# Kernel tuning notes

Measured on AMD Instinct MI355X. Metric: run time of the kernel, lower is better.

## Reference

```python
import jax, jax.numpy as jnp
import numpy as np

GROUPS = 9  # hardcoded in GTLModuleV1.forward


def setup_inputs() -> dict:
    key = jax.random.key(0)
    k1, k2, k3 = jax.random.split(key, 3)
    B, C, N, K = 4, 144, 16384, 16
    queryandkey = jax.random.normal(k1, (B, C, N), dtype=jnp.float32)
    value = jax.random.normal(k2, (B, C, N), dtype=jnp.float32)
    idx_knn = jax.random.randint(k3, (B, N, K), 0, N, dtype=jnp.int32)
    return {"queryandkey": queryandkey, "value": value, "idx_knn": idx_knn}


def _gather_neighbours(x, idx_flat, B, G, d, N, K):
    # x: (B, G, d, N); idx_flat: (B, 1, 1, N*K) -> (B, G, d, N, K)
    g = jnp.take_along_axis(x, jnp.broadcast_to(idx_flat, (B, G, d, N * K)), axis=3)
    return g.reshape(B, G, d, N, K)


def reference(queryandkey, value, idx_knn):
    B, C, N = queryandkey.shape
    K = idx_knn.shape[-1]
    G = GROUPS
    d = C // G  # Cl = C (Cnl = 0 in GTLModuleV1)

    q = queryandkey.reshape(B, G, d, N)          # LocalQuery == LocalKey source
    v = value.reshape(B, G, d, N)
    idx_flat = idx_knn.reshape(B, 1, 1, N * K)

    key_g = _gather_neighbours(q, idx_flat, B, G, d, N, K)  # (B,G,d,N,K)
    val_g = _gather_neighbours(v, idx_flat, B, G, d, N, K)  # (B,G,d,N,K)

    # LocalAtt = sum_d Q * K_gathered, softmax over neighbors
    att = jnp.einsum('bgdn,bgdnk->bgnk', q, key_g)
    att = jax.nn.softmax(att, axis=-1)                       # (B,G,N,K)

    # attention centrality: scatter_add of attention weights onto neighbor ids
    cent = jnp.zeros((B, G, N), dtype=att.dtype).at[
        jnp.arange(B)[:, None, None, None],
        jnp.arange(G)[None, :, None, None],
        idx_knn[:, None, :, :],
    ].add(att)                                               # (B,G,N)

    # weighted aggregation of gathered values
    feat = jnp.einsum('bgnk,bgdnk->bgdn', att, val_g).reshape(B, C, N)
    return feat, cent
```

## Files before the change

kernel.cpp:

```cpp
#include <hip/hip_runtime.h>
#include <hip/hip_fp16.h>

#define BATCH 4
#define CHAN  144
#define NPTS  16384
#define KNN   16
#define GRP   9
#define DIM   16
#define ROWU  (GRP * DIM)
#define PCHUNK 21
#define NPAIR (BATCH * GRP)

#define TT 32

typedef __attribute__((ext_vector_type(2))) _Float16 h2v;
typedef __attribute__((ext_vector_type(4))) float f4v;
typedef __attribute__((ext_vector_type(4))) int   i4v;
__device__ __forceinline__ h2v as_h2(unsigned int u) {
  union { unsigned int u; h2v h; } c; c.u = u; return c.h;
}

template<int J>
__device__ __forceinline__ int ibcast(int v) {
  return __builtin_amdgcn_update_dpp(0, v, (J) * 0x55, 0xF, 0xF, true);
}
template<int C>
__device__ __forceinline__ float fxor(float x) {
  int r = __builtin_amdgcn_update_dpp(0, __builtin_bit_cast(int, x), C, 0xF, 0xF, true);
  return __builtin_bit_cast(float, r);
}

__global__ __launch_bounds__(256) void pack_qv_kernel(
    const float* __restrict__ q, const float* __restrict__ v,
    unsigned int* __restrict__ qvT) {
  __shared__ float tq[TT][TT + 1];
  __shared__ float tv[TT][TT + 1];
  const int b = blockIdx.z;
  const float* qb = q + (size_t)b * CHAN * NPTS;
  const float* vb = v + (size_t)b * CHAN * NPTS;
  unsigned int* out = qvT + (size_t)b * NPTS * ROWU;
  const int n0 = blockIdx.x * TT;
  const int c0 = blockIdx.y * TT;
  const int t = threadIdx.x;

  {
    const int cl = t >> 3, nq = (t & 7) * 4;
    const int c = c0 + cl;
    if (c < CHAN) {
      const float4 a = *(const float4*)&qb[(size_t)c * NPTS + n0 + nq];
      tq[cl][nq + 0] = a.x; tq[cl][nq + 1] = a.y;
      tq[cl][nq + 2] = a.z; tq[cl][nq + 3] = a.w;
      const float4 w = *(const float4*)&vb[(size_t)c * NPTS + n0 + nq];
      tv[cl][nq + 0] = w.x; tv[cl][nq + 1] = w.y;
      tv[cl][nq + 2] = w.z; tv[cl][nq + 3] = w.w;
    }
  }
  __syncthreads();
  {
    const int nl = t >> 3, cq = (t & 7) * 4;
    const int c = c0 + cq;
    if (c < CHAN) {
      const int g = c >> 4, r = c & 15;
      __half2 k01 = __halves2half2(__float2half_rn(tq[cq + 0][nl]),
                                   __float2half_rn(tq[cq + 1][nl]));
      __half2 v01 = __halves2half2(__float2half_rn(tv[cq + 0][nl]),
                                   __float2half_rn(tv[cq + 1][nl]));
      __half2 k23 = __halves2half2(__float2half_rn(tq[cq + 2][nl]),
                                   __float2half_rn(tq[cq + 3][nl]));
      __half2 v23 = __halves2half2(__float2half_rn(tv[cq + 2][nl]),
                                   __float2half_rn(tv[cq + 3][nl]));
      *(uint4*)&out[(size_t)(n0 + nl) * ROWU + g * 16 + r] =
          make_uint4(*(unsigned int*)&k01, *(unsigned int*)&v01,
                     *(unsigned int*)&k23, *(unsigned int*)&v23);
    }
  }
}

__global__ __launch_bounds__(512, 4) void gtl_kernel(
    const unsigned int* __restrict__ qvT,
    const int*   __restrict__ idx,
    float* __restrict__ feat,
    float* __restrict__ part)
{
  const int i = blockIdx.x;
  const int x = i & 7, sblk = i >> 3;
  if (sblk >= 94 + ((x & 1) ^ 1)) return;
  int pair, chunk;
  if (sblk < 84) { pair = x + 8 * (sblk / PCHUNK); chunk = sblk % PCHUNK; }
  else           { pair = 32 + (x >> 1); chunk = (sblk - 84) + 11 * (x & 1); }
  const int b = pair / GRP;
  const int g = pair - b * GRP;

  __shared__ float lcent[NPTS];
  const int tid = threadIdx.x;

  f4v* l4 = (f4v*)lcent;
  #pragma unroll
  for (int ii = 0; ii < NPTS / 4 / 512; ++ii)
    l4[ii * 512 + tid] = (f4v){0.f, 0.f, 0.f, 0.f};
  __syncthreads();

  const int ngroups = 6 + (chunk < 2 ? 1 : 0);
  const int gstart  = 6 * chunk + (chunk < 2 ? chunk : 2);

  const int lane = tid & 63;
  const int wv   = tid >> 6;
  const int slot = lane >> 2;
  const int d    = lane & 3;

  const char* qvb  = (const char*)qvT + (size_t)b * NPTS * (ROWU * 4);
  const char* idxB = (const char*)idx + (size_t)b * NPTS * (KNN * 4);
  const unsigned laneB  = (unsigned)(g * 64 + d * 16);
  const unsigned idxoff = (unsigned)(d * 16);

  int n = gstart * 128 + wv * 16 + slot;
  i4v idq = __builtin_nontemporal_load(
      (const i4v*)(idxB + (unsigned)n * 64u + idxoff));
  uint4 qq = *(const uint4*)(qvb + (unsigned)n * (ROWU * 4u) + laneB);

  for (int it = 0; it < ngroups; ++it) {
    const h2v q01 = as_h2(qq.x);
    const h2v q23 = as_h2(qq.z);

    uint4 kvp[KNN];
#define GSTEP(K)                                                             \
    {                                                                        \
      const int mk = ibcast<((K) >> 2)>(                                     \
          ((K) & 3) == 0 ? idq.x : ((K) & 3) == 1 ? idq.y                    \
                         : ((K) & 3) == 2 ? idq.z : idq.w);                  \
      kvp[K] = *(const uint4*)(qvb + (unsigned)mk * (ROWU * 4u) + laneB);    \
    }
    GSTEP(0)  GSTEP(1)  GSTEP(2)  GSTEP(3)
    GSTEP(4)  GSTEP(5)  GSTEP(6)  GSTEP(7)
    GSTEP(8)  GSTEP(9)  GSTEP(10) GSTEP(11)
    GSTEP(12) GSTEP(13) GSTEP(14) GSTEP(15)
#undef GSTEP

    const int itn = (it + 1 < ngroups) ? it + 1 : it;
    const int nn = (gstart + itn) * 128 + wv * 16 + slot;
    const i4v idqn = __builtin_nontemporal_load(
        (const i4v*)(idxB + (unsigned)nn * 64u + idxoff));
    const uint4 qqn = *(const uint4*)(qvb + (unsigned)nn * (ROWU * 4u) + laneB);

    __builtin_amdgcn_sched_barrier(0);

    float p[KNN];
    float sum = 0.f, a0 = 0.f, a1 = 0.f, a2 = 0.f, a3 = 0.f;
#define CSTEP(K)                                                             \
    {                                                                        \
      float s = __builtin_amdgcn_fdot2(as_h2(kvp[K].x), q01, 0.f, false);    \
      s = __builtin_amdgcn_fdot2(as_h2(kvp[K].z), q23, s, false);            \
      s += fxor<0xB1>(s);                                                    \
      s += fxor<0x4E>(s);                                                    \
      const float e = __expf(s);                                             \
      p[K] = e; sum += e;                                                    \
      const float2 v01 = __half22float2(*(const __half2*)&kvp[K].y);         \
      const float2 v23 = __half22float2(*(const __half2*)&kvp[K].w);         \
      a0 += e * v01.x; a1 += e * v01.y; a2 += e * v23.x; a3 += e * v23.y;    \
    }
    CSTEP(0)  CSTEP(1)  CSTEP(2)  CSTEP(3)
    CSTEP(4)  CSTEP(5)  CSTEP(6)  CSTEP(7)
    CSTEP(8)  CSTEP(9)  CSTEP(10) CSTEP(11)
    CSTEP(12) CSTEP(13) CSTEP(14) CSTEP(15)
#undef CSTEP

    const float inv = 1.f / sum;

    const float w0 = (d == 0 ? p[0] : d == 1 ? p[4] : d == 2 ? p[8]  : p[12]) * inv;
    const float w1 = (d == 0 ? p[1] : d == 1 ? p[5] : d == 2 ? p[9]  : p[13]) * inv;
    const float w2 = (d == 0 ? p[2] : d == 1 ? p[6] : d == 2 ? p[10] : p[14]) * inv;
    const float w3 = (d == 0 ? p[3] : d == 1 ? p[7] : d == 2 ? p[11] : p[15]) * inv;
    atomicAdd(&lcent[idq.x], w0);
    atomicAdd(&lcent[idq.y], w1);
    atomicAdd(&lcent[idq.z], w2);
    atomicAdd(&lcent[idq.w], w3);

    float* fb = feat + ((size_t)b * CHAN + g * DIM + 4 * d) * NPTS + n;
    __builtin_nontemporal_store(a0 * inv, fb);
    __builtin_nontemporal_store(a1 * inv, fb + NPTS);
    __builtin_nontemporal_store(a2 * inv, fb + 2 * NPTS);
    __builtin_nontemporal_store(a3 * inv, fb + 3 * NPTS);

    n = nn; idq = idqn; qq = qqn;
  }

  __syncthreads();
  f4v* p4 = (f4v*)(part + ((size_t)pair * PCHUNK + chunk) * NPTS);
  #pragma unroll
  for (int i2 = 0; i2 < NPTS / 4 / 512; ++i2)
    __builtin_nontemporal_store(l4[i2 * 512 + tid], &p4[i2 * 512 + tid]);
}

__global__ __launch_bounds__(256) void reduce_cent_kernel(
    const float* __restrict__ part, float* __restrict__ cent) {
  const int t = blockIdx.x * 256 + threadIdx.x;
  const int bg = t >> 12;
  const int m4 = (t & 4095) << 2;
  const f4v* p = (const f4v*)(part + ((size_t)bg * PCHUNK) * NPTS + m4);
  f4v s = (f4v){0.f, 0.f, 0.f, 0.f};
  #pragma unroll
  for (int i = 0; i < PCHUNK; ++i) {
    f4v xv = __builtin_nontemporal_load(&p[(size_t)i * (NPTS / 4)]);
    s += xv;
  }
  *(f4v*)(cent + (size_t)bg * NPTS + m4) = s;
}

extern "C" void kernel_launch(void* const* d_in, const int* in_sizes, int n_in,
                              void* d_out, int out_size, void* d_ws, size_t ws_size,
                              hipStream_t stream) {
  const float* q   = (const float*)d_in[0];
  const float* v   = (const float*)d_in[1];
  const int*   idx = (const int*)d_in[2];

  float* feat = (float*)d_out;
  float* cent = feat + (size_t)BATCH * CHAN * NPTS;

  unsigned int* qvT = (unsigned int*)d_ws;
  float* part = (float*)(qvT + (size_t)BATCH * NPTS * ROWU);

  dim3 tg(NPTS / TT, (CHAN + TT - 1) / TT, BATCH);
  pack_qv_kernel<<<tg, 256, 0, stream>>>(q, v, qvT);

  gtl_kernel<<<760, 512, 0, stream>>>(qvT, idx, feat, part);

  reduce_cent_kernel<<<(NPAIR * NPTS / 4) / 256, 256, 0, stream>>>(part, cent);
}
```

Baseline: 226.5 us.

## Replace partial-centrality buffer and reduce kernel with global atomic accumulation

New measurement: 234.3 us. 3.4% more time.

```diff
diff --git a/kernel.cpp b/kernel.cpp
--- a/kernel.cpp
+++ b/kernel.cpp
@@ -8,7 +8,7 @@
 #define GRP   9
 #define DIM   16
 #define ROWU  (GRP * DIM)
-#define PCHUNK 21
+#define PCHUNK 32
 #define NPAIR (BATCH * GRP)
 
 #define TT 32
@@ -80,14 +80,13 @@
     const unsigned int* __restrict__ qvT,
     const int*   __restrict__ idx,
     float* __restrict__ feat,
-    float* __restrict__ part)
+    float* __restrict__ cent)
 {
   const int i = blockIdx.x;
   const int x = i & 7, sblk = i >> 3;
-  if (sblk >= 94 + ((x & 1) ^ 1)) return;
   int pair, chunk;
-  if (sblk < 84) { pair = x + 8 * (sblk / PCHUNK); chunk = sblk % PCHUNK; }
-  else           { pair = 32 + (x >> 1); chunk = (sblk - 84) + 11 * (x & 1); }
+  if (sblk < 128) { pair = x + 8 * (sblk >> 5); chunk = sblk & 31; }
+  else            { pair = 32 + (x >> 1); chunk = (sblk - 128) + 16 * (x & 1); }
   const int b = pair / GRP;
   const int g = pair - b * GRP;
 
@@ -100,8 +99,8 @@
     l4[ii * 512 + tid] = (f4v){0.f, 0.f, 0.f, 0.f};
   __syncthreads();
 
-  const int ngroups = 6 + (chunk < 2 ? 1 : 0);
-  const int gstart  = 6 * chunk + (chunk < 2 ? chunk : 2);
+  const int NG = 4;
+  const int gstart = 4 * chunk;
 
   const int lane = tid & 63;
   const int wv   = tid >> 6;
@@ -118,7 +117,7 @@
       (const i4v*)(idxB + (unsigned)n * 64u + idxoff));
   uint4 qq = *(const uint4*)(qvb + (unsigned)n * (ROWU * 4u) + laneB);
 
-  for (int it = 0; it < ngroups; ++it) {
+  for (int it = 0; it < NG; ++it) {
     const h2v q01 = as_h2(qq.x);
     const h2v q23 = as_h2(qq.z);
 
@@ -136,7 +135,7 @@
     GSTEP(12) GSTEP(13) GSTEP(14) GSTEP(15)
 #undef GSTEP
 
-    const int itn = (it + 1 < ngroups) ? it + 1 : it;
+    const int itn = (it + 1 < NG) ? it + 1 : it;
     const int nn = (gstart + itn) * 128 + wv * 16 + slot;
     const i4v idqn = __builtin_nontemporal_load(
         (const i4v*)(idxB + (unsigned)nn * 64u + idxoff));
@@ -185,25 +184,10 @@
   }
 
   __syncthreads();
-  f4v* p4 = (f4v*)(part + ((size_t)pair * PCHUNK + chunk) * NPTS);
+  float* cb = cent + (size_t)pair * NPTS;
   #pragma unroll
-  for (int i2 = 0; i2 < NPTS / 4 / 512; ++i2)
-    __builtin_nontemporal_store(l4[i2 * 512 + tid], &p4[i2 * 512 + tid]);
-}
-
-__global__ __launch_bounds__(256) void reduce_cent_kernel(
-    const float* __restrict__ part, float* __restrict__ cent) {
-  const int t = blockIdx.x * 256 + threadIdx.x;
-  const int bg = t >> 12;
-  const int m4 = (t & 4095) << 2;
-  const f4v* p = (const f4v*)(part + ((size_t)bg * PCHUNK) * NPTS + m4);
-  f4v s = (f4v){0.f, 0.f, 0.f, 0.f};
-  #pragma unroll
-  for (int i = 0; i < PCHUNK; ++i) {
-    f4v xv = __builtin_nontemporal_load(&p[(size_t)i * (NPTS / 4)]);
-    s += xv;
-  }
-  *(f4v*)(cent + (size_t)bg * NPTS + m4) = s;
+  for (int ii = 0; ii < NPTS / 512; ++ii)
+    atomicAdd(&cb[ii * 512 + tid], lcent[ii * 512 + tid]);
 }
 
 extern "C" void kernel_launch(void* const* d_in, const int* in_sizes, int n_in,
@@ -217,12 +201,11 @@
   float* cent = feat + (size_t)BATCH * CHAN * NPTS;
 
   unsigned int* qvT = (unsigned int*)d_ws;
-  float* part = (float*)(qvT + (size_t)BATCH * NPTS * ROWU);
+
+  hipMemsetAsync(cent, 0, (size_t)NPAIR * NPTS * sizeof(float), stream);
 
   dim3 tg(NPTS / TT, (CHAN + TT - 1) / TT, BATCH);
   pack_qv_kernel<<<tg, 256, 0, stream>>>(q, v, qvT);
 
-  gtl_kernel<<<760, 512, 0, stream>>>(qvT, idx, feat, part);
-
-  reduce_cent_kernel<<<(NPAIR * NPTS / 4) / 256, 256, 0, stream>>>(part, cent);
-}
+  gtl_kernel<<<NPAIR * PCHUNK, 512, 0, stream>>>(qvT, idx, feat, cent);
+}
```
